# Optimization experiments

Hardware: AMD Instinct MI355X
Metric: run time of the kernel (lower is better)

## Reference

```python
import jax, jax.numpy as jnp
import numpy as np

D_STATE = 64
HEADDIM = 64
D_CONV = 4
EPS = 1e-5


def _layernorm(x, w, b):
    m = jnp.mean(x, -1, keepdims=True)
    v = jnp.mean((x - m) ** 2, -1, keepdims=True)
    return (x - m) * jax.lax.rsqrt(v + EPS) * w + b


def _mamba2(x, W_in, conv_w, conv_b, dt_bias, A_log, Dh, rms_w, W_out):
    # Mamba2 (SSD) forward: in_proj -> causal depthwise conv + silu -> selective scan
    # -> gated RMSNorm -> out_proj.  ngroups=1, headdim=64, d_state=64.
    Bb, L, _ = x.shape
    d_inner = rms_w.shape[0]
    H = dt_bias.shape[0]
    P = d_inner // H
    conv_dim = d_inner + 2 * D_STATE
    zxbcdt = x @ W_in                                   # [B,L,2*d_inner+2*N+H]
    z = zxbcdt[..., :d_inner]
    xBC = zxbcdt[..., d_inner:d_inner + conv_dim]
    dt = zxbcdt[..., d_inner + conv_dim:]               # [B,L,H]
    # causal depthwise conv1d (kernel D_CONV) + bias + silu
    xpad = jnp.pad(xBC, ((0, 0), (D_CONV - 1, 0), (0, 0)))
    xBC = sum(conv_w[k] * xpad[:, k:k + L] for k in range(D_CONV)) + conv_b
    xBC = jax.nn.silu(xBC)
    xh = xBC[..., :d_inner].reshape(Bb, L, H, P)        # [B,L,H,P]
    Bm = xBC[..., d_inner:d_inner + D_STATE]            # [B,L,N]
    Cm = xBC[..., d_inner + D_STATE:]                   # [B,L,N]
    dt = jax.nn.softplus(dt + dt_bias)                  # [B,L,H]
    A = -jnp.exp(A_log)                                 # [H]
    da = jnp.exp(dt * A)                                # [B,L,H] discrete decay
    dtx = dt[..., None] * xh                            # [B,L,H,P]

    def step(h, inp):
        da_t, dtx_t, B_t, C_t = inp
        h = da_t[:, :, None, None] * h + jnp.einsum('bhp,bn->bhpn', dtx_t, B_t)
        y_t = jnp.einsum('bhpn,bn->bhp', h, C_t)
        return h, y_t

    h0 = jnp.zeros((Bb, H, P, D_STATE), x.dtype)
    _, y = jax.lax.scan(step, h0, (da.transpose(1, 0, 2), dtx.transpose(1, 0, 2, 3),
                                   Bm.transpose(1, 0, 2), Cm.transpose(1, 0, 2)))
    y = y.transpose(1, 0, 2, 3) + Dh[None, None, :, None] * xh   # skip term
    y = y.reshape(Bb, L, d_inner)
    # gated RMSNorm (norm_before_gate=False): rmsnorm(y * silu(z)) * weight
    y = y * jax.nn.silu(z)
    y = y * jax.lax.rsqrt(jnp.mean(y * y, -1, keepdims=True) + EPS) * rms_w
    return y @ W_out


def _mamba_params(key, d_model, pre):
    d_inner = 2 * d_model
    H = d_inner // HEADDIM
    conv_dim = d_inner + 2 * D_STATE
    d_in = 2 * d_inner + 2 * D_STATE + H
    k = jax.random.split(key, 5)
    return {
        pre + '_W_in': jax.random.normal(k[0], (d_model, d_in), jnp.float32) * (d_model ** -0.5),
        pre + '_conv_w': jax.random.normal(k[1], (D_CONV, conv_dim), jnp.float32) * 0.2,
        pre + '_conv_b': jnp.zeros((conv_dim,), jnp.float32),
        pre + '_dt_bias': jnp.log(jnp.expm1(jax.random.uniform(k[2], (H,), jnp.float32, 0.001, 0.1))),
        pre + '_A_log': jnp.log(jax.random.uniform(k[3], (H,), jnp.float32, 1.0, 16.0)),
        pre + '_D': jnp.ones((H,), jnp.float32),
        pre + '_rms_w': jnp.ones((d_inner,), jnp.float32),
        pre + '_W_out': jax.random.normal(k[4], (d_inner, d_model), jnp.float32) * (d_inner ** -0.5),
    }


def setup_inputs() -> dict:
    key = jax.random.key(0)
    ks = jax.random.split(key, 3)
    B, L, C = 8, 1024, 128
    inp = {'x': jax.random.normal(ks[0], (B, L, C), jnp.float32)}
    inp['ln_spa_w'] = jnp.ones((C,), jnp.float32)
    inp['ln_spa_b'] = jnp.zeros((C,), jnp.float32)
    inp['ln_spe_w'] = jnp.ones((L,), jnp.float32)
    inp['ln_spe_b'] = jnp.zeros((L,), jnp.float32)
    inp.update(_mamba_params(ks[1], C, 'spa'))
    inp.update(_mamba_params(ks[2], L, 'spe'))
    return inp


def reference(x, ln_spa_w, ln_spa_b, ln_spe_w, ln_spe_b,
              spa_W_in, spa_conv_w, spa_conv_b, spa_dt_bias, spa_A_log, spa_D, spa_rms_w, spa_W_out,
              spe_W_in, spe_conv_w, spe_conv_b, spe_dt_bias, spe_A_log, spe_D, spe_rms_w, spe_W_out):
    # SSD_Block.forward (drop_path=0 -> identity)
    x_spa = _layernorm(x, ln_spa_w, ln_spa_b)
    x_spa = _mamba2(x_spa, spa_W_in, spa_conv_w, spa_conv_b, spa_dt_bias,
                    spa_A_log, spa_D, spa_rms_w, spa_W_out) + x
    x_spe = x_spa.transpose(0, 2, 1)                      # [B,C,L]
    x_spe = _layernorm(x_spe, ln_spe_w, ln_spe_b)
    x_spe = _mamba2(x_spe, spe_W_in, spe_conv_w, spe_conv_b, spe_dt_bias,
                    spe_A_log, spe_D, spe_rms_w, spe_W_out)
    return x_spe.transpose(0, 2, 1) + x_spa
```

## Files before the change

kernel.cpp:

```cpp
#include <hip/hip_runtime.h>
#include <hip/hip_bf16.h>

#define EPSV 1e-5f

typedef __attribute__((ext_vector_type(8))) short short8v;
typedef __attribute__((ext_vector_type(4))) float f32x4;

__device__ inline unsigned short f2bf(float f) {
  __hip_bfloat16 h = __float2bfloat16(f);
  return *reinterpret_cast<unsigned short*>(&h);
}

__device__ inline float siluf(float x) { return x / (1.f + expf(-x)); }

__device__ inline float block_sum(float v, float* lds) {
  #pragma unroll
  for (int o = 32; o; o >>= 1) v += __shfl_xor(v, o);
  int tid = threadIdx.x;
  if ((tid & 63) == 0) lds[tid >> 6] = v;
  __syncthreads();
  float r = lds[0] + lds[1] + lds[2] + lds[3];
  __syncthreads();
  return r;
}

__device__ inline float wave_prefix_incl(float v, int lane) {
  #pragma unroll
  for (int o = 1; o < 64; o <<= 1) {
    float u = __shfl_up(v, o);
    if (lane >= o) v += u;
  }
  return v;
}

__device__ inline void wtconv_tile(const float* __restrict__ W,
                                   unsigned short* __restrict__ Wt,
                                   int K, int N, int bx, int by) {
  __shared__ float tile[64][65];
  int n0 = bx * 64, k0 = by * 64;
  int tid = threadIdx.x;
  int r = tid >> 4, c4 = (tid & 15) * 4;
  #pragma unroll
  for (int i = 0; i < 4; i++) {
    int kk = r + i * 16;
    float4 v = make_float4(0.f, 0.f, 0.f, 0.f);
    if (n0 + c4 < N) v = *reinterpret_cast<const float4*>(&W[(long)(k0 + kk) * N + n0 + c4]);
    tile[kk][c4] = v.x; tile[kk][c4 + 1] = v.y; tile[kk][c4 + 2] = v.z; tile[kk][c4 + 3] = v.w;
  }
  __syncthreads();
  #pragma unroll
  for (int i = 0; i < 4; i++) {
    int nl = r + i * 16;
    if (n0 + nl < N) {
      ushort4 o;
      o.x = f2bf(tile[c4 + 0][nl]);
      o.y = f2bf(tile[c4 + 1][nl]);
      o.z = f2bf(tile[c4 + 2][nl]);
      o.w = f2bf(tile[c4 + 3][nl]);
      *reinterpret_cast<ushort4*>(&Wt[(long)(n0 + nl) * K + k0 + c4]) = o;
    }
  }
}

__global__ __launch_bounds__(256) void ln_wt_fused(const float* __restrict__ x,
                                                   const float* __restrict__ w,
                                                   const float* __restrict__ bb,
                                                   unsigned short* __restrict__ outA,
                                                   const float* __restrict__ W0,
                                                   unsigned short* __restrict__ T0,
                                                   const float* __restrict__ W1,
                                                   unsigned short* __restrict__ T1,
                                                   const float* __restrict__ W2,
                                                   unsigned short* __restrict__ T2,
                                                   const float* __restrict__ W3,
                                                   unsigned short* __restrict__ T3) {
  int id = blockIdx.x;
  if (id < 4096) {
    int tid = threadIdx.x;
    __shared__ float lds[4];
    long row = (long)id * 2 + (tid >> 7);
    int lane = tid & 127;
    int base = (tid >> 7) << 1;
    float v = x[row * 128 + lane];
    float s = v;
    #pragma unroll
    for (int o = 32; o; o >>= 1) s += __shfl_xor(s, o);
    if ((tid & 63) == 0) lds[tid >> 6] = s;
    __syncthreads();
    float m = (lds[base] + lds[base + 1]) * (1.f / 128.f);
    float d = v - m;
    float q = d * d;
    #pragma unroll
    for (int o = 32; o; o >>= 1) q += __shfl_xor(q, o);
    __syncthreads();
    if ((tid & 63) == 0) lds[tid >> 6] = q;
    __syncthreads();
    float inv = rsqrtf((lds[base] + lds[base + 1]) * (1.f / 128.f) + EPSV);
    outA[row * 128 + lane] = f2bf(d * inv * w[lane] + bb[lane]);
  } else {
    id -= 4096;
    if (id < 22)        { int r = id;        wtconv_tile(W0, T0, 128,  644,  r % 11, r / 11); }
    else if (id < 30)   { int r = id - 22;   wtconv_tile(W1, T1, 256,  128,  r % 2,  r / 2); }
    else if (id < 1102) { int r = id - 30;   wtconv_tile(W2, T2, 1024, 4256, r % 67, r / 67); }
    else                { int r = id - 1102; wtconv_tile(W3, T3, 2048, 1024, r % 16, r / 16); }
  }
}

__global__ __launch_bounds__(256) void spe_normT(const float* __restrict__ xspa,
                                                 const float* __restrict__ part2,
                                                 const float* __restrict__ w,
                                                 const float* __restrict__ bb,
                                                 unsigned short* __restrict__ out) {
  __shared__ float tile[128][65];
  int c0 = blockIdx.x * 64, l0 = blockIdx.y * 128, b = blockIdx.z;
  int tid = threadIdx.x;
  int rr = tid >> 4, c4 = (tid & 15) * 4;
  #pragma unroll
  for (int p = 0; p < 8; p++) {
    int l = rr + p * 16;
    f32x4 v = *reinterpret_cast<const f32x4*>(
        &xspa[((long)b * 1024 + l0 + l) * 128 + c0 + c4]);
    tile[l][c4] = v[0]; tile[l][c4 + 1] = v[1];
    tile[l][c4 + 2] = v[2]; tile[l][c4 + 3] = v[3];
  }
  __syncthreads();
  int ch = tid >> 2, lq = tid & 3;
  int gc = c0 + ch;
  int bx = gc >> 6, cl = gc & 63;
  float ssum = 0.f, qsum = 0.f;
  #pragma unroll
  for (int sub = 0; sub < 16; sub++) {
    int by = b * 16 + sub;
    float2 pq = *reinterpret_cast<const float2*>(&part2[(((by * 2 + bx) * 64) + cl) * 2]);
    ssum += pq.x; qsum += pq.y;
  }
  float mm = ssum * (1.f / 1024.f);
  float rstd = rsqrtf(qsum * (1.f / 1024.f) - mm * mm + EPSV);
  #pragma unroll
  for (int j = 0; j < 8; j++) {
    int qidx = lq + j * 4;
    int l = qidx * 4;
    float4 wv = *reinterpret_cast<const float4*>(&w[l0 + l]);
    float4 bv = *reinterpret_cast<const float4*>(&bb[l0 + l]);
    ushort4 o;
    o.x = f2bf((tile[l + 0][ch] - mm) * rstd * wv.x + bv.x);
    o.y = f2bf((tile[l + 1][ch] - mm) * rstd * wv.y + bv.y);
    o.z = f2bf((tile[l + 2][ch] - mm) * rstd * wv.z + bv.z);
    o.w = f2bf((tile[l + 3][ch] - mm) * rstd * wv.w + bv.w);
    *reinterpret_cast<ushort4*>(&out[((long)b * 128 + c0 + ch) * 1024 + l0 + l]) = o;
  }
}

__global__ __launch_bounds__(256) void gemm128_split(const unsigned short* __restrict__ A,
                                                     const unsigned short* __restrict__ Bt,
                                                     float* __restrict__ out,
                                                     float* __restrict__ o2,
                                                     float* __restrict__ o3,
                                                     int M, int N, int K,
                                                     int c1, int c2) {
  __shared__ unsigned short As[128 * 40];
  __shared__ unsigned short Bs[128 * 40];
  int tid = threadIdx.x;
  int lane = tid & 63, w = tid >> 6;
  int wr = (w >> 1) * 64, wc = (w & 1) * 64;
  int ln15 = lane & 15, kg = lane >> 4;
  int rowBase = blockIdx.y * 128, colBase = blockIdx.x * 128;
  int sr = tid >> 1, sk = (tid & 1) * 16;
  f32x4 acc[4][4] = {};
  for (int k0 = 0; k0 < K; k0 += 32) {
    {
      const unsigned short* ap = &A[(long)(rowBase + sr) * K + k0 + sk];
      short8v a0 = *reinterpret_cast<const short8v*>(ap);
      short8v a1 = *reinterpret_cast<const short8v*>(ap + 8);
      *reinterpret_cast<short8v*>(&As[sr * 40 + sk]) = a0;
      *reinterpret_cast<short8v*>(&As[sr * 40 + sk + 8]) = a1;
      int n = colBase + sr;
      short8v b0 = {0, 0, 0, 0, 0, 0, 0, 0}, b1 = b0;
      if (n < N) {
        const unsigned short* bp = &Bt[(long)n * K + k0 + sk];
        b0 = *reinterpret_cast<const short8v*>(bp);
        b1 = *reinterpret_cast<const short8v*>(bp + 8);
      }
      *reinterpret_cast<short8v*>(&Bs[sr * 40 + sk]) = b0;
      *reinterpret_cast<short8v*>(&Bs[sr * 40 + sk + 8]) = b1;
    }
    __syncthreads();
    short8v af[4], bfr[4];
    #pragma unroll
    for (int mt = 0; mt < 4; mt++)
      af[mt] = *reinterpret_cast<const short8v*>(&As[(wr + mt * 16 + ln15) * 40 + kg * 8]);
    #pragma unroll
    for (int nt = 0; nt < 4; nt++)
      bfr[nt] = *reinterpret_cast<const short8v*>(&Bs[(wc + nt * 16 + ln15) * 40 + kg * 8]);
    #pragma unroll
    for (int mt = 0; mt < 4; mt++)
      #pragma unroll
      for (int nt = 0; nt < 4; nt++)
        acc[mt][nt] = __builtin_amdgcn_mfma_f32_16x16x32_bf16(af[mt], bfr[nt], acc[mt][nt], 0, 0, 0);
    __syncthreads();
  }
  #pragma unroll
  for (int mt = 0; mt < 4; mt++)
    #pragma unroll
    for (int nt = 0; nt < 4; nt++)
      #pragma unroll
      for (int q = 0; q < 4; q++) {
        int r = rowBase + wr + mt * 16 + kg * 4 + q;
        int c = colBase + wc + nt * 16 + ln15;
        if (c < N) {
          float v = acc[mt][nt][q];
          if (c < c1) out[(long)r * c1 + c] = v;
          else if (c < c2) o2[(long)r * (c2 - c1) + (c - c1)] = v;
          else o3[(long)r * (N - c2) + (c - c2)] = v;
        }
      }
}

template <int MODE>
__global__ __launch_bounds__(256) void gemm_mfma(const unsigned short* __restrict__ A,
                                                 const unsigned short* __restrict__ Bt,
                                                 const float* __restrict__ R,
                                                 float* __restrict__ out,
                                                 float* __restrict__ part2,
                                                 int M, int N, int K) {
  __shared__ unsigned short As[64 * 40];
  __shared__ unsigned short Bs[64 * 40];
  int tid = threadIdx.x;
  int lane = tid & 63, w = tid >> 6;
  int wr = (w >> 1) * 32, wc = (w & 1) * 32;
  int ln15 = lane & 15, kg = lane >> 4;
  int rowBase = blockIdx.y * 64, colBase = blockIdx.x * 64;
  int sm = tid >> 2, skb = (tid & 3) * 8;
  f32x4 acc[2][2] = {};
  for (int k0 = 0; k0 < K; k0 += 32) {
    {
      short8v av = *reinterpret_cast<const short8v*>(&A[(long)(rowBase + sm) * K + k0 + skb]);
      *reinterpret_cast<short8v*>(&As[sm * 40 + skb]) = av;
      int n = colBase + sm;
      short8v bv = {0, 0, 0, 0, 0, 0, 0, 0};
      if (n < N) bv = *reinterpret_cast<const short8v*>(&Bt[(long)n * K + k0 + skb]);
      *reinterpret_cast<short8v*>(&Bs[sm * 40 + skb]) = bv;
    }
    __syncthreads();
    short8v af[2], bfr[2];
    #pragma unroll
    for (int mt = 0; mt < 2; mt++)
      af[mt] = *reinterpret_cast<const short8v*>(&As[(wr + mt * 16 + ln15) * 40 + kg * 8]);
    #pragma unroll
    for (int nt = 0; nt < 2; nt++)
      bfr[nt] = *reinterpret_cast<const short8v*>(&Bs[(wc + nt * 16 + ln15) * 40 + kg * 8]);
    #pragma unroll
    for (int mt = 0; mt < 2; mt++)
      #pragma unroll
      for (int nt = 0; nt < 2; nt++)
        acc[mt][nt] = __builtin_amdgcn_mfma_f32_16x16x32_bf16(af[mt], bfr[nt], acc[mt][nt], 0, 0, 0);
    __syncthreads();
  }
  if (MODE == 1) {
    float sC[2] = {0.f, 0.f}, qC[2] = {0.f, 0.f};
    #pragma unroll
    for (int mt = 0; mt < 2; mt++)
      #pragma unroll
      for (int nt = 0; nt < 2; nt++)
        #pragma unroll
        for (int q = 0; q < 4; q++) {
          int r = rowBase + wr + mt * 16 + kg * 4 + q;
          int c = colBase + wc + nt * 16 + ln15;
          float v = acc[mt][nt][q] + R[(long)r * N + c];
          out[(long)r * N + c] = v;
          sC[nt] += v;
          qC[nt] += v * v;
        }
    __shared__ float redS[4][32], redQ[4][32];
    #pragma unroll
    for (int nt = 0; nt < 2; nt++) {
      sC[nt] += __shfl_xor(sC[nt], 16);
      sC[nt] += __shfl_xor(sC[nt], 32);
      qC[nt] += __shfl_xor(qC[nt], 16);
      qC[nt] += __shfl_xor(qC[nt], 32);
    }
    if (lane < 16) {
      redS[w][ln15] = sC[0];       redQ[w][ln15] = qC[0];
      redS[w][16 + ln15] = sC[1];  redQ[w][16 + ln15] = qC[1];
    }
    __syncthreads();
    if (tid < 64) {
      int c = tid;
      int grp = c >> 5, lo = c & 31;
      float ss = redS[grp][lo] + redS[grp + 2][lo];
      float qq = redQ[grp][lo] + redQ[grp + 2][lo];
      long slot = ((long)(blockIdx.y * 2 + blockIdx.x) * 64 + c) * 2;
      part2[slot] = ss;
      part2[slot + 1] = qq;
    }
  } else {
    #pragma unroll
    for (int mt = 0; mt < 2; mt++)
      #pragma unroll
      for (int nt = 0; nt < 2; nt++)
        #pragma unroll
        for (int q = 0; q < 4; q++) {
          int r = rowBase + wr + mt * 16 + kg * 4 + q;
          int c = colBase + wc + nt * 16 + ln15;
          if (c < N) {
            int bb = r >> 7, ch = r & 127;
            out[(long)bb * 131072 + (long)c * 128 + ch] =
                acc[mt][nt][q] + R[((long)bb * 1024 + c) * 128 + ch];
          }
        }
  }
}

__global__ __launch_bounds__(256) void conv_dtda(const float* __restrict__ zx,
                                                 const float* __restrict__ cw,
                                                 const float* __restrict__ cb,
                                                 float* __restrict__ cout,
                                                 const float* __restrict__ raw,
                                                 const float* __restrict__ dtbias,
                                                 const float* __restrict__ alog,
                                                 float* __restrict__ dt,
                                                 float* __restrict__ la,
                                                 int Bb, int L, int conv_dim,
                                                 int H, int rowsH, int convBlocks) {
  int tid = threadIdx.x;
  if ((int)blockIdx.x < convBlocks) {
    long idx4 = (long)blockIdx.x * 256 + tid;
    int nch4 = conv_dim >> 2;
    long total4 = (long)Bb * L * nch4;
    if (idx4 >= total4) return;
    int ch = (int)(idx4 % nch4) << 2;
    long rt = idx4 / nch4;
    int t = (int)(rt % L);
    int b = (int)(rt / L);
    f32x4 acc = *reinterpret_cast<const f32x4*>(&cb[ch]);
    #pragma unroll
    for (int k = 0; k < 4; k++) {
      int tt = t + k - 3;
      if (tt >= 0) {
        f32x4 wv = *reinterpret_cast<const f32x4*>(&cw[k * conv_dim + ch]);
        f32x4 zv = *reinterpret_cast<const f32x4*>(
            &zx[((long)b * L + tt) * conv_dim + ch]);
        acc += wv * zv;
      }
    }
    f32x4 o;
    o[0] = siluf(acc[0]); o[1] = siluf(acc[1]);
    o[2] = siluf(acc[2]); o[3] = siluf(acc[3]);
    *reinterpret_cast<f32x4*>(&cout[rt * conv_dim + ch]) = o;
  } else {
    int idx = ((int)blockIdx.x - convBlocks) * 256 + tid;
    if (idx >= rowsH) return;
    int h = idx % H;
    float v = raw[idx] + dtbias[h];
    float sp = (v > 20.f) ? v : log1pf(expf(v));
    dt[idx] = sp;
    la[idx] = -expf(alog[h]) * sp;
  }
}

__global__ __launch_bounds__(256) void ssd_local(const float* __restrict__ xbc,
                                                 const float* __restrict__ dtv,
                                                 const float* __restrict__ la,
                                                 float* __restrict__ Sc,
                                                 float* __restrict__ Aprod,
                                                 int NC, int nc_launch, int H,
                                                 int conv_dim, int d_inner) {
  int blk = blockIdx.x;
  int c = blk % nc_launch, bh = blk / nc_launch;
  int h = bh % H, b = bh / H;
  int tid = threadIdx.x;
  long row0 = ((long)(b * NC + c)) * 64;
  __shared__ unsigned short XpT[64 * 72];
  __shared__ unsigned short BT[64 * 72];
  __shared__ float Ws[64];
  int tq = tid >> 4, cq = (tid & 15) << 2;
  f32x4 xr[4], br[4];
  #pragma unroll
  for (int i = 0; i < 4; i++) {
    int t = tq + i * 16;
    const float* rp = xbc + (row0 + t) * conv_dim;
    xr[i] = *reinterpret_cast<const f32x4*>(rp + (h << 6) + cq);
    br[i] = *reinterpret_cast<const f32x4*>(rp + d_inner + cq);
  }
  if (tid < 64) {
    long r = (row0 + tid) * H + h;
    float cum = wave_prefix_incl(la[r], tid);
    float cT = __shfl(cum, 63);
    Ws[tid] = expf(cT - cum) * dtv[r];
    if (tid == 63) Aprod[(long)bh * NC + c] = expf(cT);
  }
  __syncthreads();
  #pragma unroll
  for (int i = 0; i < 4; i++) {
    int t = tq + i * 16;
    float wv = Ws[t];
    #pragma unroll
    for (int j = 0; j < 4; j++) {
      XpT[(cq + j) * 72 + t] = f2bf(wv * xr[i][j]);
      BT[(cq + j) * 72 + t] = f2bf(br[i][j]);
    }
  }
  __syncthreads();
  int lane = tid & 63, wv2 = tid >> 6;
  int wr = (wv2 >> 1) * 32, wc = (wv2 & 1) * 32;
  int ln15 = lane & 15, kg = lane >> 4;
  f32x4 acc[2][2] = {};
  #pragma unroll
  for (int ks = 0; ks < 2; ks++) {
    short8v af[2], bq[2];
    #pragma unroll
    for (int mt = 0; mt < 2; mt++)
      af[mt] = *reinterpret_cast<const short8v*>(&XpT[(wr + mt * 16 + ln15) * 72 + ks * 32 + kg * 8]);
    #pragma unroll
    for (int nt = 0; nt < 2; nt++)
      bq[nt] = *reinterpret_cast<const short8v*>(&BT[(wc + nt * 16 + ln15) * 72 + ks * 32 + kg * 8]);
    #pragma unroll
    for (int mt = 0; mt < 2; mt++)
      #pragma unroll
      for (int nt = 0; nt < 2; nt++)
        acc[mt][nt] = __builtin_amdgcn_mfma_f32_16x16x32_bf16(af[mt], bq[nt], acc[mt][nt], 0, 0, 0);
  }
  float* base = Sc + ((long)bh * NC + c) * 4096;
  #pragma unroll
  for (int mt = 0; mt < 2; mt++)
    #pragma unroll
    for (int nt = 0; nt < 2; nt++)
      #pragma unroll
      for (int q = 0; q < 4; q++) {
        int p = wr + mt * 16 + kg * 4 + q;
        int n = wc + nt * 16 + ln15;
        base[p * 64 + n] = acc[mt][nt][q];
      }
}

__global__ __launch_bounds__(256) void ssd_out(const float* __restrict__ xbc,
                                               const float* __restrict__ dtv,
                                               const float* __restrict__ la,
                                               const float* __restrict__ Sc,
                                               const float* __restrict__ Aprod,
                                               const float* __restrict__ Dvec,
                                               float* __restrict__ y,
                                               int NC, int H, int conv_dim,
                                               int d_inner) {
  int blk = blockIdx.x;
  int c = blk % NC, bh = blk / NC;
  int h = bh % H, b = bh / H;
  int tid = threadIdx.x;
  long row0 = ((long)(b * NC + c)) * 64;
  __shared__ unsigned short Cb[64 * 72];
  __shared__ unsigned short Bb[64 * 72];
  __shared__ unsigned short XT[64 * 72];
  __shared__ unsigned short hb[64 * 72];
  __shared__ float Cum[64], Dt[64];
  int tq = tid >> 4, cq = (tid & 15) << 2;
  #pragma unroll
  for (int i = 0; i < 4; i++) {
    int t = tq + i * 16;
    const float* rp = xbc + (row0 + t) * conv_dim;
    f32x4 cvv = *reinterpret_cast<const f32x4*>(rp + d_inner + 64 + cq);
    f32x4 bvv = *reinterpret_cast<const f32x4*>(rp + d_inner + cq);
    f32x4 xvv = *reinterpret_cast<const f32x4*>(rp + (h << 6) + cq);
    ushort4 co, bo;
    co.x = f2bf(cvv[0]); co.y = f2bf(cvv[1]); co.z = f2bf(cvv[2]); co.w = f2bf(cvv[3]);
    bo.x = f2bf(bvv[0]); bo.y = f2bf(bvv[1]); bo.z = f2bf(bvv[2]); bo.w = f2bf(bvv[3]);
    *reinterpret_cast<ushort4*>(&Cb[t * 72 + cq]) = co;
    *reinterpret_cast<ushort4*>(&Bb[t * 72 + cq]) = bo;
    #pragma unroll
    for (int j = 0; j < 4; j++) XT[(cq + j) * 72 + t] = f2bf(xvv[j]);
  }
  if (c > 0) {
    f32x4 hreg[4] = {};
    const float* ap = Aprod + (long)bh * NC;
    for (int j = 0; j < c; j++) {
      const float* sb = Sc + ((long)bh * NC + j) * 4096;
      float a = ap[j];
      #pragma unroll
      for (int i = 0; i < 4; i++) {
        int p = tq + i * 16;
        f32x4 sv = *reinterpret_cast<const f32x4*>(&sb[p * 64 + cq]);
        hreg[i] = hreg[i] * a + sv;
      }
    }
    #pragma unroll
    for (int i = 0; i < 4; i++) {
      int p = tq + i * 16;
      ushort4 ho;
      ho.x = f2bf(hreg[i][0]); ho.y = f2bf(hreg[i][1]);
      ho.z = f2bf(hreg[i][2]); ho.w = f2bf(hreg[i][3]);
      *reinterpret_cast<ushort4*>(&hb[p * 72 + cq]) = ho;
    }
  }
  if (tid < 64) {
    long r = (row0 + tid) * H + h;
    Cum[tid] = wave_prefix_incl(la[r], tid);
    Dt[tid] = dtv[r];
  }
  __syncthreads();
  int lane = tid & 63, wv2 = tid >> 6;
  int wr = (wv2 >> 1) * 32, wc = (wv2 & 1) * 32;
  int ln15 = lane & 15, kg = lane >> 4;
  f32x4 accA[2][2] = {};
  #pragma unroll
  for (int ks = 0; ks < 2; ks++) {
    short8v af[2], bq[2];
    #pragma unroll
    for (int mt = 0; mt < 2; mt++)
      af[mt] = *reinterpret_cast<const short8v*>(&Cb[(wr + mt * 16 + ln15) * 72 + ks * 32 + kg * 8]);
    #pragma unroll
    for (int nt = 0; nt < 2; nt++)
      bq[nt] = *reinterpret_cast<const short8v*>(&Bb[(wc + nt * 16 + ln15) * 72 + ks * 32 + kg * 8]);
    #pragma unroll
    for (int mt = 0; mt < 2; mt++)
      #pragma unroll
      for (int nt = 0; nt < 2; nt++)
        accA[mt][nt] = __builtin_amdgcn_mfma_f32_16x16x32_bf16(af[mt], bq[nt], accA[mt][nt], 0, 0, 0);
  }
  unsigned short gmb[2][2][4];
  #pragma unroll
  for (int mt = 0; mt < 2; mt++)
    #pragma unroll
    for (int nt = 0; nt < 2; nt++)
      #pragma unroll
      for (int q = 0; q < 4; q++) {
        int t = wr + mt * 16 + kg * 4 + q;
        int s = wc + nt * 16 + ln15;
        float v = (s <= t) ? accA[mt][nt][q] * expf(Cum[t] - Cum[s]) * Dt[s] : 0.f;
        gmb[mt][nt][q] = f2bf(v);
      }
  __syncthreads();
  #pragma unroll
  for (int mt = 0; mt < 2; mt++)
    #pragma unroll
    for (int nt = 0; nt < 2; nt++)
      #pragma unroll
      for (int q = 0; q < 4; q++)
        Bb[(wr + mt * 16 + kg * 4 + q) * 72 + wc + nt * 16 + ln15] = gmb[mt][nt][q];
  __syncthreads();
  f32x4 accY[2][2] = {}, accZ[2][2] = {};
  #pragma unroll
  for (int ks = 0; ks < 2; ks++) {
    short8v af[2], bq[2];
    #pragma unroll
    for (int mt = 0; mt < 2; mt++)
      af[mt] = *reinterpret_cast<const short8v*>(&Bb[(wr + mt * 16 + ln15) * 72 + ks * 32 + kg * 8]);
    #pragma unroll
    for (int nt = 0; nt < 2; nt++)
      bq[nt] = *reinterpret_cast<const short8v*>(&XT[(wc + nt * 16 + ln15) * 72 + ks * 32 + kg * 8]);
    #pragma unroll
    for (int mt = 0; mt < 2; mt++)
      #pragma unroll
      for (int nt = 0; nt < 2; nt++)
        accY[mt][nt] = __builtin_amdgcn_mfma_f32_16x16x32_bf16(af[mt], bq[nt], accY[mt][nt], 0, 0, 0);
  }
  if (c > 0) {
    #pragma unroll
    for (int ks = 0; ks < 2; ks++) {
      short8v af[2], bq[2];
      #pragma unroll
      for (int mt = 0; mt < 2; mt++)
        af[mt] = *reinterpret_cast<const short8v*>(&Cb[(wr + mt * 16 + ln15) * 72 + ks * 32 + kg * 8]);
      #pragma unroll
      for (int nt = 0; nt < 2; nt++)
        bq[nt] = *reinterpret_cast<const short8v*>(&hb[(wc + nt * 16 + ln15) * 72 + ks * 32 + kg * 8]);
      #pragma unroll
      for (int mt = 0; mt < 2; mt++)
        #pragma unroll
        for (int nt = 0; nt < 2; nt++)
          accZ[mt][nt] = __builtin_amdgcn_mfma_f32_16x16x32_bf16(af[mt], bq[nt], accZ[mt][nt], 0, 0, 0);
    }
  }
  float Dv = Dvec[h];
  #pragma unroll
  for (int mt = 0; mt < 2; mt++)
    #pragma unroll
    for (int q = 0; q < 4; q++) {
      int t = wr + mt * 16 + kg * 4 + q;
      float wB = expf(Cum[t]);
      const float* xp = xbc + (row0 + t) * conv_dim + (h << 6);
      float* yp = y + (row0 + t) * d_inner + (h << 6);
      #pragma unroll
      for (int nt = 0; nt < 2; nt++) {
        int p = wc + nt * 16 + ln15;
        yp[p] = accY[mt][nt][q] + accZ[mt][nt][q] * wB + xp[p] * Dv;
      }
    }
}

template <int NJ>
__global__ __launch_bounds__(256) void gate_rms_bf16(const float* __restrict__ y,
                                                     const float* __restrict__ z,
                                                     const float* __restrict__ rmsw,
                                                     unsigned short* __restrict__ ab,
                                                     int d_inner) {
  long row = blockIdx.x;
  const float* yr = y + row * d_inner;
  const float* zr = z + row * d_inner;
  __shared__ float lds[4];
  float g[NJ];
  float ss = 0.f;
  #pragma unroll
  for (int j = 0; j < NJ; j++) {
    int c = threadIdx.x + (j << 8);
    float gv = yr[c] * siluf(zr[c]);
    g[j] = gv;
    ss += gv * gv;
  }
  float tot = block_sum(ss, lds);
  float inv = rsqrtf(tot / (float)d_inner + EPSV);
  #pragma unroll
  for (int j = 0; j < NJ; j++) {
    int c = threadIdx.x + (j << 8);
    ab[row * d_inner + c] = f2bf(g[j] * inv * rmsw[c]);
  }
}

extern "C" void kernel_launch(void* const* d_in, const int* in_sizes, int n_in,
                              void* d_out, int out_size, void* d_ws,
                              size_t ws_size, hipStream_t stream) {
  const float* x        = (const float*)d_in[0];
  const float* ln_spa_w = (const float*)d_in[1];
  const float* ln_spa_b = (const float*)d_in[2];
  const float* ln_spe_w = (const float*)d_in[3];
  const float* ln_spe_b = (const float*)d_in[4];
  const float* spa_W_in   = (const float*)d_in[5];
  const float* spa_conv_w = (const float*)d_in[6];
  const float* spa_conv_b = (const float*)d_in[7];
  const float* spa_dt_b   = (const float*)d_in[8];
  const float* spa_A_log  = (const float*)d_in[9];
  const float* spa_D      = (const float*)d_in[10];
  const float* spa_rms_w  = (const float*)d_in[11];
  const float* spa_W_out  = (const float*)d_in[12];
  const float* spe_W_in   = (const float*)d_in[13];
  const float* spe_conv_w = (const float*)d_in[14];
  const float* spe_conv_b = (const float*)d_in[15];
  const float* spe_dt_b   = (const float*)d_in[16];
  const float* spe_A_log  = (const float*)d_in[17];
  const float* spe_D      = (const float*)d_in[18];
  const float* spe_rms_w  = (const float*)d_in[19];
  const float* spe_W_out  = (const float*)d_in[20];
  float* out = (float*)d_out;

  float* ws = (float*)d_ws;
  float* xspa   = ws;
  float* z      = ws + 1048576;
  float* xbcraw = ws + 3145728;
  float* dtraw  = ws + 6291456;
  float* cv     = ws + 6324224;
  float* dtb    = ws + 9469952;
  float* la     = ws + 9502720;
  float* yb     = ws + 9535488;
  unsigned short* Abf     = (unsigned short*)(ws + 11634688);
  unsigned short* Wt_spai = (unsigned short*)(ws + 12683264);
  unsigned short* Wt_spao = (unsigned short*)(ws + 12724480);
  unsigned short* Wt_spei = (unsigned short*)(ws + 12740864);
  unsigned short* Wt_speo = (unsigned short*)(ws + 14919936);

  hipLaunchKernelGGL(ln_wt_fused, dim3(5710), dim3(256), 0, stream,
                     x, ln_spa_w, ln_spa_b, Abf,
                     spa_W_in, Wt_spai, spa_W_out, Wt_spao,
                     spe_W_in, Wt_spei, spe_W_out, Wt_speo);

  hipLaunchKernelGGL(gemm128_split, dim3(6, 64), dim3(256), 0, stream,
                     Abf, Wt_spai, z, xbcraw, dtraw,
                     8192, 644, 128, 256, 640);
  hipLaunchKernelGGL(conv_dtda, dim3(3200), dim3(256), 0, stream,
                     xbcraw, spa_conv_w, spa_conv_b, cv,
                     dtraw, spa_dt_b, spa_A_log, dtb, la,
                     8, 1024, 384, 4, 32768, 3072);
  hipLaunchKernelGGL(ssd_local, dim3(480), dim3(256), 0, stream,
                     cv, dtb, la, xbcraw, dtraw, 16, 15, 4, 384, 256);
  hipLaunchKernelGGL(ssd_out, dim3(512), dim3(256), 0, stream,
                     cv, dtb, la, xbcraw, dtraw, spa_D, yb, 16, 4, 384, 256);
  hipLaunchKernelGGL((gate_rms_bf16<1>), dim3(8192), dim3(256), 0, stream,
                     yb, z, spa_rms_w, Abf, 256);
  hipLaunchKernelGGL((gemm_mfma<1>), dim3(2, 128), dim3(256), 0, stream,
                     Abf, Wt_spao, x, xspa, dtb, 8192, 128, 256);

  hipLaunchKernelGGL(spe_normT, dim3(2, 8, 8), dim3(256), 0, stream,
                     xspa, dtb, ln_spe_w, ln_spe_b, Abf);
  hipLaunchKernelGGL(gemm128_split, dim3(34, 8), dim3(256), 0, stream,
                     Abf, Wt_spei, z, xbcraw, dtraw,
                     1024, 4256, 1024, 2048, 4224);
  hipLaunchKernelGGL(conv_dtda, dim3(2304), dim3(256), 0, stream,
                     xbcraw, spe_conv_w, spe_conv_b, cv,
                     dtraw, spe_dt_b, spe_A_log, dtb, la,
                     8, 128, 2176, 32, 32768, 2176);
  hipLaunchKernelGGL(ssd_local, dim3(256), dim3(256), 0, stream,
                     cv, dtb, la, xbcraw, dtraw, 2, 1, 32, 2176, 2048);
  hipLaunchKernelGGL(ssd_out, dim3(512), dim3(256), 0, stream,
                     cv, dtb, la, xbcraw, dtraw, spe_D, yb, 2, 32, 2176, 2048);
  hipLaunchKernelGGL((gate_rms_bf16<8>), dim3(1024), dim3(256), 0, stream,
                     yb, z, spe_rms_w, Abf, 2048);
  hipLaunchKernelGGL((gemm_mfma<2>), dim3(16, 16), dim3(256), 0, stream,
                     Abf, Wt_speo, xspa, out, nullptr, 1024, 1024, 2048);
}
```

Baseline: 177.5 us.

## Store SSD intermediates in bf16 and use direct global-to-LDS loads in GEMM

The gate tensor z, the post-conv activations and the scan output y are now stored as bf16 instead of fp32, which roughly halves memory traffic for the conv, SSD and gated-RMSNorm kernels. The split GEMM now stages its A and B tiles with global_load_lds straight into unpadded LDS. This drops the register round-trip and the N bounds check, so padded columns read past the weight rows. gate_rms is rewritten to handle one row per wavefront with vectorised loads and a shuffle-only reduction. The costs are bf16 rounding of intermediates, possible LDS bank conflicts now that the padding is gone, and out-of-range weight reads in the last column tile.

After: 173.7 us. 2.2% less time.

```diff
diff --git a/kernel.cpp b/kernel.cpp
--- a/kernel.cpp
+++ b/kernel.cpp
@@ -11,7 +11,17 @@
   return *reinterpret_cast<unsigned short*>(&h);
 }
 
+__device__ inline float bf2f(unsigned short u) {
+  return __uint_as_float(((unsigned int)u) << 16);
+}
+
 __device__ inline float siluf(float x) { return x / (1.f + expf(-x)); }
+
+__device__ inline void gload_lds16(const void* g, void* l) {
+  __builtin_amdgcn_global_load_lds(
+      (const __attribute__((address_space(1))) void*)g,
+      (__attribute__((address_space(3))) void*)l, 16, 0, 0);
+}
 
 __device__ inline float block_sum(float v, float* lds) {
   #pragma unroll
@@ -153,45 +163,34 @@
 
 __global__ __launch_bounds__(256) void gemm128_split(const unsigned short* __restrict__ A,
                                                      const unsigned short* __restrict__ Bt,
-                                                     float* __restrict__ out,
+                                                     unsigned short* __restrict__ zout,
                                                      float* __restrict__ o2,
                                                      float* __restrict__ o3,
                                                      int M, int N, int K,
                                                      int c1, int c2) {
-  __shared__ unsigned short As[128 * 40];
-  __shared__ unsigned short Bs[128 * 40];
+  __shared__ unsigned short As[128 * 32];
+  __shared__ unsigned short Bs[128 * 32];
   int tid = threadIdx.x;
   int lane = tid & 63, w = tid >> 6;
   int wr = (w >> 1) * 64, wc = (w & 1) * 64;
   int ln15 = lane & 15, kg = lane >> 4;
   int rowBase = blockIdx.y * 128, colBase = blockIdx.x * 128;
-  int sr = tid >> 1, sk = (tid & 1) * 16;
+  int srow = w * 32 + (lane >> 2);
+  int scol = (lane & 3) * 8;
   f32x4 acc[4][4] = {};
   for (int k0 = 0; k0 < K; k0 += 32) {
-    {
-      const unsigned short* ap = &A[(long)(rowBase + sr) * K + k0 + sk];
-      short8v a0 = *reinterpret_cast<const short8v*>(ap);
-      short8v a1 = *reinterpret_cast<const short8v*>(ap + 8);
-      *reinterpret_cast<short8v*>(&As[sr * 40 + sk]) = a0;
-      *reinterpret_cast<short8v*>(&As[sr * 40 + sk + 8]) = a1;
-      int n = colBase + sr;
-      short8v b0 = {0, 0, 0, 0, 0, 0, 0, 0}, b1 = b0;
-      if (n < N) {
-        const unsigned short* bp = &Bt[(long)n * K + k0 + sk];
-        b0 = *reinterpret_cast<const short8v*>(bp);
-        b1 = *reinterpret_cast<const short8v*>(bp + 8);
-      }
-      *reinterpret_cast<short8v*>(&Bs[sr * 40 + sk]) = b0;
-      *reinterpret_cast<short8v*>(&Bs[sr * 40 + sk + 8]) = b1;
-    }
+    gload_lds16(&A[(long)(rowBase + srow) * K + k0 + scol], &As[(w * 32) * 32]);
+    gload_lds16(&A[(long)(rowBase + srow + 16) * K + k0 + scol], &As[(w * 32 + 16) * 32]);
+    gload_lds16(&Bt[(long)(colBase + srow) * K + k0 + scol], &Bs[(w * 32) * 32]);
+    gload_lds16(&Bt[(long)(colBase + srow + 16) * K + k0 + scol], &Bs[(w * 32 + 16) * 32]);
     __syncthreads();
     short8v af[4], bfr[4];
     #pragma unroll
     for (int mt = 0; mt < 4; mt++)
-      af[mt] = *reinterpret_cast<const short8v*>(&As[(wr + mt * 16 + ln15) * 40 + kg * 8]);
+      af[mt] = *reinterpret_cast<const short8v*>(&As[(wr + mt * 16 + ln15) * 32 + kg * 8]);
     #pragma unroll
     for (int nt = 0; nt < 4; nt++)
-      bfr[nt] = *reinterpret_cast<const short8v*>(&Bs[(wc + nt * 16 + ln15) * 40 + kg * 8]);
+      bfr[nt] = *reinterpret_cast<const short8v*>(&Bs[(wc + nt * 16 + ln15) * 32 + kg * 8]);
     #pragma unroll
     for (int mt = 0; mt < 4; mt++)
       #pragma unroll
@@ -209,7 +208,7 @@
         int c = colBase + wc + nt * 16 + ln15;
         if (c < N) {
           float v = acc[mt][nt][q];
-          if (c < c1) out[(long)r * c1 + c] = v;
+          if (c < c1) zout[(long)r * c1 + c] = f2bf(v);
           else if (c < c2) o2[(long)r * (c2 - c1) + (c - c1)] = v;
           else o3[(long)r * (N - c2) + (c - c2)] = v;
         }
@@ -314,7 +313,7 @@
 __global__ __launch_bounds__(256) void conv_dtda(const float* __restrict__ zx,
                                                  const float* __restrict__ cw,
                                                  const float* __restrict__ cb,
-                                                 float* __restrict__ cout,
+                                                 unsigned short* __restrict__ cout,
                                                  const float* __restrict__ raw,
                                                  const float* __restrict__ dtbias,
                                                  const float* __restrict__ alog,
@@ -343,10 +342,10 @@
         acc += wv * zv;
       }
     }
-    f32x4 o;
-    o[0] = siluf(acc[0]); o[1] = siluf(acc[1]);
-    o[2] = siluf(acc[2]); o[3] = siluf(acc[3]);
-    *reinterpret_cast<f32x4*>(&cout[rt * conv_dim + ch]) = o;
+    ushort4 o;
+    o.x = f2bf(siluf(acc[0])); o.y = f2bf(siluf(acc[1]));
+    o.z = f2bf(siluf(acc[2])); o.w = f2bf(siluf(acc[3]));
+    *reinterpret_cast<ushort4*>(&cout[rt * conv_dim + ch]) = o;
   } else {
     int idx = ((int)blockIdx.x - convBlocks) * 256 + tid;
     if (idx >= rowsH) return;
@@ -358,7 +357,7 @@
   }
 }
 
-__global__ __launch_bounds__(256) void ssd_local(const float* __restrict__ xbc,
+__global__ __launch_bounds__(256) void ssd_local(const unsigned short* __restrict__ xbc,
                                                  const float* __restrict__ dtv,
                                                  const float* __restrict__ la,
                                                  float* __restrict__ Sc,
@@ -374,13 +373,13 @@
   __shared__ unsigned short BT[64 * 72];
   __shared__ float Ws[64];
   int tq = tid >> 4, cq = (tid & 15) << 2;
-  f32x4 xr[4], br[4];
+  ushort4 xr[4], br[4];
   #pragma unroll
   for (int i = 0; i < 4; i++) {
     int t = tq + i * 16;
-    const float* rp = xbc + (row0 + t) * conv_dim;
-    xr[i] = *reinterpret_cast<const f32x4*>(rp + (h << 6) + cq);
-    br[i] = *reinterpret_cast<const f32x4*>(rp + d_inner + cq);
+    const unsigned short* rp = xbc + (row0 + t) * conv_dim;
+    xr[i] = *reinterpret_cast<const ushort4*>(rp + (h << 6) + cq);
+    br[i] = *reinterpret_cast<const ushort4*>(rp + d_inner + cq);
   }
   if (tid < 64) {
     long r = (row0 + tid) * H + h;
@@ -394,11 +393,14 @@
   for (int i = 0; i < 4; i++) {
     int t = tq + i * 16;
     float wv = Ws[t];
-    #pragma unroll
-    for (int j = 0; j < 4; j++) {
-      XpT[(cq + j) * 72 + t] = f2bf(wv * xr[i][j]);
-      BT[(cq + j) * 72 + t] = f2bf(br[i][j]);
-    }
+    XpT[(cq + 0) * 72 + t] = f2bf(wv * bf2f(xr[i].x));
+    XpT[(cq + 1) * 72 + t] = f2bf(wv * bf2f(xr[i].y));
+    XpT[(cq + 2) * 72 + t] = f2bf(wv * bf2f(xr[i].z));
+    XpT[(cq + 3) * 72 + t] = f2bf(wv * bf2f(xr[i].w));
+    BT[(cq + 0) * 72 + t] = br[i].x;
+    BT[(cq + 1) * 72 + t] = br[i].y;
+    BT[(cq + 2) * 72 + t] = br[i].z;
+    BT[(cq + 3) * 72 + t] = br[i].w;
   }
   __syncthreads();
   int lane = tid & 63, wv2 = tid >> 6;
@@ -433,13 +435,13 @@
       }
 }
 
-__global__ __launch_bounds__(256) void ssd_out(const float* __restrict__ xbc,
+__global__ __launch_bounds__(256) void ssd_out(const unsigned short* __restrict__ xbc,
                                                const float* __restrict__ dtv,
                                                const float* __restrict__ la,
                                                const float* __restrict__ Sc,
                                                const float* __restrict__ Aprod,
                                                const float* __restrict__ Dvec,
-                                               float* __restrict__ y,
+                                               unsigned short* __restrict__ y,
                                                int NC, int H, int conv_dim,
                                                int d_inner) {
   int blk = blockIdx.x;
@@ -456,17 +458,16 @@
   #pragma unroll
   for (int i = 0; i < 4; i++) {
     int t = tq + i * 16;
-    const float* rp = xbc + (row0 + t) * conv_dim;
-    f32x4 cvv = *reinterpret_cast<const f32x4*>(rp + d_inner + 64 + cq);
-    f32x4 bvv = *reinterpret_cast<const f32x4*>(rp + d_inner + cq);
-    f32x4 xvv = *reinterpret_cast<const f32x4*>(rp + (h << 6) + cq);
-    ushort4 co, bo;
-    co.x = f2bf(cvv[0]); co.y = f2bf(cvv[1]); co.z = f2bf(cvv[2]); co.w = f2bf(cvv[3]);
-    bo.x = f2bf(bvv[0]); bo.y = f2bf(bvv[1]); bo.z = f2bf(bvv[2]); bo.w = f2bf(bvv[3]);
-    *reinterpret_cast<ushort4*>(&Cb[t * 72 + cq]) = co;
-    *reinterpret_cast<ushort4*>(&Bb[t * 72 + cq]) = bo;
-    #pragma unroll
-    for (int j = 0; j < 4; j++) XT[(cq + j) * 72 + t] = f2bf(xvv[j]);
+    const unsigned short* rp = xbc + (row0 + t) * conv_dim;
+    ushort4 cu = *reinterpret_cast<const ushort4*>(rp + d_inner + 64 + cq);
+    ushort4 bu = *reinterpret_cast<const ushort4*>(rp + d_inner + cq);
+    ushort4 xu = *reinterpret_cast<const ushort4*>(rp + (h << 6) + cq);
+    *reinterpret_cast<ushort4*>(&Cb[t * 72 + cq]) = cu;
+    *reinterpret_cast<ushort4*>(&Bb[t * 72 + cq]) = bu;
+    XT[(cq + 0) * 72 + t] = xu.x;
+    XT[(cq + 1) * 72 + t] = xu.y;
+    XT[(cq + 2) * 72 + t] = xu.z;
+    XT[(cq + 3) * 72 + t] = xu.w;
   }
   if (c > 0) {
     f32x4 hreg[4] = {};
@@ -576,41 +577,53 @@
     for (int q = 0; q < 4; q++) {
       int t = wr + mt * 16 + kg * 4 + q;
       float wB = expf(Cum[t]);
-      const float* xp = xbc + (row0 + t) * conv_dim + (h << 6);
-      float* yp = y + (row0 + t) * d_inner + (h << 6);
+      const unsigned short* xp = xbc + (row0 + t) * conv_dim + (h << 6);
+      unsigned short* yp = y + (row0 + t) * d_inner + (h << 6);
       #pragma unroll
       for (int nt = 0; nt < 2; nt++) {
         int p = wc + nt * 16 + ln15;
-        yp[p] = accY[mt][nt][q] + accZ[mt][nt][q] * wB + xp[p] * Dv;
+        yp[p] = f2bf(accY[mt][nt][q] + accZ[mt][nt][q] * wB + bf2f(xp[p]) * Dv);
       }
     }
 }
 
-template <int NJ>
-__global__ __launch_bounds__(256) void gate_rms_bf16(const float* __restrict__ y,
-                                                     const float* __restrict__ z,
+template <int CPL>
+__global__ __launch_bounds__(256) void gate_rms_bf16(const unsigned short* __restrict__ y,
+                                                     const unsigned short* __restrict__ z,
                                                      const float* __restrict__ rmsw,
                                                      unsigned short* __restrict__ ab,
                                                      int d_inner) {
-  long row = blockIdx.x;
-  const float* yr = y + row * d_inner;
-  const float* zr = z + row * d_inner;
-  __shared__ float lds[4];
-  float g[NJ];
+  long row = (long)blockIdx.x * 4 + (threadIdx.x >> 6);
+  int lane = threadIdx.x & 63;
+  const unsigned short* yr = y + row * d_inner;
+  const unsigned short* zr = z + row * d_inner;
+  float g[CPL];
   float ss = 0.f;
   #pragma unroll
-  for (int j = 0; j < NJ; j++) {
-    int c = threadIdx.x + (j << 8);
-    float gv = yr[c] * siluf(zr[c]);
-    g[j] = gv;
-    ss += gv * gv;
-  }
-  float tot = block_sum(ss, lds);
-  float inv = rsqrtf(tot / (float)d_inner + EPSV);
-  #pragma unroll
-  for (int j = 0; j < NJ; j++) {
-    int c = threadIdx.x + (j << 8);
-    ab[row * d_inner + c] = f2bf(g[j] * inv * rmsw[c]);
+  for (int j = 0; j < CPL / 4; j++) {
+    int c = j * 256 + lane * 4;
+    ushort4 yv = *reinterpret_cast<const ushort4*>(&yr[c]);
+    ushort4 zv = *reinterpret_cast<const ushort4*>(&zr[c]);
+    float g0 = bf2f(yv.x) * siluf(bf2f(zv.x));
+    float g1 = bf2f(yv.y) * siluf(bf2f(zv.y));
+    float g2 = bf2f(yv.z) * siluf(bf2f(zv.z));
+    float g3 = bf2f(yv.w) * siluf(bf2f(zv.w));
+    g[j * 4 + 0] = g0; g[j * 4 + 1] = g1; g[j * 4 + 2] = g2; g[j * 4 + 3] = g3;
+    ss += g0 * g0 + g1 * g1 + g2 * g2 + g3 * g3;
+  }
+  #pragma unroll
+  for (int o = 32; o; o >>= 1) ss += __shfl_xor(ss, o);
+  float inv = rsqrtf(ss / (float)d_inner + EPSV);
+  #pragma unroll
+  for (int j = 0; j < CPL / 4; j++) {
+    int c = j * 256 + lane * 4;
+    float4 wv = *reinterpret_cast<const float4*>(&rmsw[c]);
+    ushort4 o;
+    o.x = f2bf(g[j * 4 + 0] * inv * wv.x);
+    o.y = f2bf(g[j * 4 + 1] * inv * wv.y);
+    o.z = f2bf(g[j * 4 + 2] * inv * wv.z);
+    o.w = f2bf(g[j * 4 + 3] * inv * wv.w);
+    *reinterpret_cast<ushort4*>(&ab[row * d_inner + c]) = o;
   }
 }
 
@@ -642,13 +655,13 @@
 
   float* ws = (float*)d_ws;
   float* xspa   = ws;
-  float* z      = ws + 1048576;
+  unsigned short* z = (unsigned short*)(ws + 1048576);
   float* xbcraw = ws + 3145728;
   float* dtraw  = ws + 6291456;
-  float* cv     = ws + 6324224;
+  unsigned short* cv = (unsigned short*)(ws + 6324224);
   float* dtb    = ws + 9469952;
   float* la     = ws + 9502720;
-  float* yb     = ws + 9535488;
+  unsigned short* yb = (unsigned short*)(ws + 9535488);
   unsigned short* Abf     = (unsigned short*)(ws + 11634688);
   unsigned short* Wt_spai = (unsigned short*)(ws + 12683264);
   unsigned short* Wt_spao = (unsigned short*)(ws + 12724480);
@@ -671,7 +684,7 @@
                      cv, dtb, la, xbcraw, dtraw, 16, 15, 4, 384, 256);
   hipLaunchKernelGGL(ssd_out, dim3(512), dim3(256), 0, stream,
                      cv, dtb, la, xbcraw, dtraw, spa_D, yb, 16, 4, 384, 256);
-  hipLaunchKernelGGL((gate_rms_bf16<1>), dim3(8192), dim3(256), 0, stream,
+  hipLaunchKernelGGL((gate_rms_bf16<4>), dim3(2048), dim3(256), 0, stream,
                      yb, z, spa_rms_w, Abf, 256);
   hipLaunchKernelGGL((gemm_mfma<1>), dim3(2, 128), dim3(256), 0, stream,
                      Abf, Wt_spao, x, xspa, dtb, 8192, 128, 256);
@@ -689,7 +702,7 @@
                      cv, dtb, la, xbcraw, dtraw, 2, 1, 32, 2176, 2048);
   hipLaunchKernelGGL(ssd_out, dim3(512), dim3(256), 0, stream,
                      cv, dtb, la, xbcraw, dtraw, spe_D, yb, 2, 32, 2176, 2048);
-  hipLaunchKernelGGL((gate_rms_bf16<8>), dim3(1024), dim3(256), 0, stream,
+  hipLaunchKernelGGL((gate_rms_bf16<32>), dim3(256), dim3(256), 0, stream,
                      yb, z, spe_rms_w, Abf, 2048);
   hipLaunchKernelGGL((gemm_mfma<2>), dim3(16, 16), dim3(256), 0, stream,
                      Abf, Wt_speo, xspa, out, nullptr, 1024, 1024, 2048);
```
